# Kernel optimization log

Hardware: AMD Instinct MI355X
Metric: run time of the kernel (lower is better)

The kernel has to match this reference:

```python
import jax, jax.numpy as jnp
import numpy as np

B, C, H, W = 8, 512, 64, 64
NH = 8                 # num_heads
HD = C // NH           # head_dim = 64
WIN = 8 * 8            # tokens per window
NW = (H * W) // WIN    # number of windows = 64


def setup_inputs() -> dict:
    key = jax.random.key(0)
    ks = jax.random.split(key, 8)
    w = lambda k, shape: jax.random.normal(k, shape, jnp.float32) * 0.02
    return {
        "x": jax.random.normal(ks[0], (B, C, H, W), jnp.float32),
        "Wq": w(ks[1], (C, C)), "bq": jnp.zeros((C,), jnp.float32),
        "Wk": w(ks[2], (C, C)), "bk": jnp.zeros((C,), jnp.float32),
        "Wv": w(ks[3], (C, C)), "bv": jnp.zeros((C,), jnp.float32),
        "Bbias": w(ks[4], (WIN, WIN)),  # additive relative bias per (q,k) position in window
    }


def reference(x, Wq, bq, Wk, bk, Wv, bv, Bbias):
    shape = x.shape
    # (B, C, H, W) -> (B, n_windows, window, C)
    xw = x.reshape(shape[0], NW, WIN, C)
    # QKV projections (torch Linear: y = x @ W^T + b)
    q = (xw @ Wq.T + bq).reshape(B, NW, WIN, NH, HD).transpose(0, 1, 3, 2, 4)
    k = (xw @ Wk.T + bk).reshape(B, NW, WIN, NH, HD).transpose(0, 1, 3, 2, 4)
    v = (xw @ Wv.T + bv).reshape(B, NW, WIN, NH, HD).transpose(0, 1, 3, 2, 4)
    scale = 1.0 / jnp.sqrt(jnp.float32(HD))
    scores = jnp.einsum("bwhqd,bwhkd->bwhqk", q, k) * scale + Bbias  # bias broadcasts over b,w,h
    probs = jax.nn.softmax(scores, axis=-1)
    out = jnp.einsum("bwhqk,bwhkd->bwhqd", probs, v)
    out = out.transpose(0, 1, 3, 2, 4).reshape(shape)
    return out
```

## Files before the change

kernel.cpp:

```cpp
#include <hip/hip_runtime.h>
#include <hip/hip_bf16.h>


typedef __attribute__((ext_vector_type(8))) short bf16x8;
typedef __attribute__((ext_vector_type(4))) float f32x4;

#define GLDS(gp, lp) __builtin_amdgcn_global_load_lds( \
    (const __attribute__((address_space(1))) unsigned int*)(gp), \
    (__attribute__((address_space(3))) unsigned int*)(lp), 16, 0, 0)

__device__ __forceinline__ unsigned short f2bf(float f) {
  union { __hip_bfloat16 h; unsigned short u; } v;
  v.h = __float2bfloat16(f);
  return v.u;
}

__global__ __launch_bounds__(256) void prep_convert(
    const float* __restrict__ X, const float* __restrict__ Wq,
    const float* __restrict__ Wk, const float* __restrict__ Wv,
    unsigned short* __restrict__ Xb, unsigned short* __restrict__ Wc) {
  const unsigned int i = blockIdx.x * 256 + threadIdx.x;
  const float* src;
  unsigned short* dst;
  if (i < 2097152u) {
    src = X + (size_t)i * 8;
    dst = Xb + (size_t)i * 8;
  } else {
    const unsigned int j = i - 2097152u;
    const unsigned int e = j * 8;
    const unsigned int n = e >> 9, kk = e & 511;
    src = ((n < 512) ? Wq : (n < 1024 ? Wk : Wv)) + (size_t)(n & 511) * 512 + kk;
    dst = Wc + (size_t)n * 512 + kk;
  }
  float4 f0 = *(const float4*)(src);
  float4 f1 = *(const float4*)(src + 4);
  __align__(16) unsigned short u[8];
  u[0] = f2bf(f0.x); u[1] = f2bf(f0.y); u[2] = f2bf(f0.z); u[3] = f2bf(f0.w);
  u[4] = f2bf(f1.x); u[5] = f2bf(f1.y); u[6] = f2bf(f1.z); u[7] = f2bf(f1.w);
  *(bf16x8*)(dst) = *(const bf16x8*)(u);
}

__global__ __launch_bounds__(512, 2) void qkv_gemm_256(
    const unsigned short* __restrict__ Xb, const unsigned short* __restrict__ Wc,
    const float* __restrict__ bq, const float* __restrict__ bk,
    const float* __restrict__ bv,
    unsigned short* __restrict__ Qo, unsigned short* __restrict__ Ko,
    unsigned short* __restrict__ Vo) {
  __shared__ __align__(16) char LDS[131072];

  const int tid  = threadIdx.x;
  const int lane = tid & 63;
  const int wid  = tid >> 6;
  const int wm = wid >> 2, wn = wid & 3;

  const int work = (int)(blockIdx.x & 7) * 96 + (int)(blockIdx.x >> 3);
  const int bx = work % 6, by = work / 6;
  const int n0 = bx * 256, m0 = by * 256;

  const int lcol  = ((lane & 3) * 8) ^ ((lane >= 32) ? 16 : 0);
  const int arow0 = (wid >> 1) * 16 + (lane >> 2);
  const int acol0 = (wid & 1) * 32 + lcol;

#define STAGE_A(half, tt) do { \
    const unsigned short* g = Xb + (size_t)(m0 + (half) * 128 + arow0) * 512 + (tt) * 64 + acol0; \
    char* l = LDS + ((tt) & 1) * 32768 + (half) * 16384 + wid * 1024; \
    GLDS(g, l); \
    GLDS(g + 64 * 512, l + 8192); \
  } while (0)

#define STAGE_B(half, tt) do { \
    const unsigned short* g = Wc + (size_t)(n0 + (half) * 128 + arow0) * 512 + (tt) * 64 + acol0; \
    char* l = LDS + 65536 + ((tt) & 1) * 32768 + (half) * 16384 + wid * 1024; \
    GLDS(g, l); \
    GLDS(g + 64 * 512, l + 8192); \
  } while (0)

  const int sloff = (((lane & 15) * 64) + ((lane >> 4) * 16)) ^ ((lane & 8) ? 32 : 0);
  char* const Ab = LDS + wm * 16384 + sloff;
  char* const Bb2 = LDS + 65536 + (wn >> 1) * 16384 + sloff;
  const int bfr = (wn & 1) * 4;

  f32x4 acc[8][4];
#pragma unroll
  for (int i = 0; i < 8; ++i)
#pragma unroll
    for (int j = 0; j < 4; ++j) acc[i][j] = (f32x4){0.f, 0.f, 0.f, 0.f};

#define RD_A(dst, ks, bo) do { \
    _Pragma("unroll") for (int mi = 0; mi < 8; ++mi) \
      dst[mi] = *(const bf16x8*)(Ab + (bo) + mi * 2048 + (ks) * 1024); \
  } while (0)

#define RD_B(dst, ks, bo) do { \
    _Pragma("unroll") for (int ni = 0; ni < 4; ++ni) \
      dst[ni] = *(const bf16x8*)(Bb2 + (bo) + (bfr + ni) * 2048 + (ks) * 1024); \
  } while (0)

#define MMH(aa, bb) do { \
    _Pragma("unroll") for (int mi = 0; mi < 8; ++mi) \
    _Pragma("unroll") for (int ni = 0; ni < 4; ++ni) \
      acc[mi][ni] = __builtin_amdgcn_mfma_f32_16x16x32_bf16( \
          aa[mi], bb[ni], acc[mi][ni], 0, 0, 0); \
  } while (0)

  STAGE_A(0, 0); STAGE_A(1, 0); STAGE_B(0, 0); STAGE_B(1, 0);
  asm volatile("s_waitcnt vmcnt(0)" ::: "memory");
  __builtin_amdgcn_s_barrier();

  bf16x8 aP[8], bP[4], aQ[8], bQ[4];
  RD_A(aP, 0, 0); RD_B(bP, 0, 0);

  for (int t = 0; t < 8; ++t) {
    const int bo = (t & 1) * 32768;
    if (t + 1 < 8) {
      STAGE_A(0, t + 1); STAGE_A(1, t + 1);
      STAGE_B(0, t + 1); STAGE_B(1, t + 1);
    }
    RD_A(aQ, 1, bo); RD_B(bQ, 1, bo);
    MMH(aP, bP);
    MMH(aQ, bQ);
    if (t + 1 < 8) asm volatile("s_waitcnt vmcnt(0)" ::: "memory");
    __builtin_amdgcn_s_barrier();
    if (t + 1 < 8) { RD_A(aP, 0, bo ^ 32768); RD_B(bP, 0, bo ^ 32768); }
  }

  {
    const int p = n0 >> 9;
    const float* bias = (p == 0) ? bq : (p == 1) ? bk : bv;
    const float qs = (p == 0) ? 0.125f : 1.0f;
    const int hi = lane >> 4, lr = lane & 15;
    const int h = ((n0 & 511) + wn * 64) >> 6;
    char* const scr = LDS + wid * 8192;
    float bsv[4];
#pragma unroll
    for (int ni = 0; ni < 4; ++ni)
      bsv[ni] = bias[(n0 & 511) + wn * 64 + ni * 16 + lr];

#pragma unroll
    for (int wh = 0; wh < 2; ++wh) {
      asm volatile("s_waitcnt lgkmcnt(0)" ::: "memory");
      __builtin_amdgcn_sched_barrier(0);
      if (p < 2) {
#pragma unroll
        for (int f = 0; f < 4; ++f)
#pragma unroll
          for (int ni = 0; ni < 4; ++ni) {
            const int d = ni * 16 + lr;
#pragma unroll
            for (int rr = 0; rr < 4; ++rr) {
              const int t = f * 16 + hi * 4 + rr;
              const int off = t * 64 + (d ^ ((t & 7) << 3));
              *(unsigned short*)(scr + off * 2) =
                  f2bf((acc[wh * 4 + f][ni][rr] + bsv[ni]) * qs);
            }
          }
      } else {
#pragma unroll
        for (int f = 0; f < 4; ++f)
#pragma unroll
          for (int ni = 0; ni < 4; ++ni) {
            const int d = ni * 16 + lr;
            const int t0 = f * 16 + hi * 4;
            ushort4 pk;
            pk.x = f2bf(acc[wh * 4 + f][ni][0] + bsv[ni]);
            pk.y = f2bf(acc[wh * 4 + f][ni][1] + bsv[ni]);
            pk.z = f2bf(acc[wh * 4 + f][ni][2] + bsv[ni]);
            pk.w = f2bf(acc[wh * 4 + f][ni][3] + bsv[ni]);
            const int off = d * 64 + (t0 ^ ((d & 7) << 3));
            *(ushort4*)(scr + off * 2) = pk;
          }
      }
      asm volatile("s_waitcnt lgkmcnt(0)" ::: "memory");
      __builtin_amdgcn_sched_barrier(0);
      const int win = (m0 + wm * 128 + wh * 64) >> 6;
      unsigned short* dst =
          ((p == 0) ? Qo : (p == 1) ? Ko : Vo) + (size_t)(win * 8 + h) * 4096;
#pragma unroll
      for (int i = 0; i < 8; ++i) {
        const int r = i * 8 + (lane >> 3);
        const int c = lane & 7;
        const int off = r * 64 + ((c ^ (r & 7)) * 8);
        bf16x8 row = *(const bf16x8*)(scr + off * 2);
        *(bf16x8*)(dst + r * 64 + c * 8) = row;
      }
    }
  }
#undef STAGE_A
#undef STAGE_B
#undef RD_A
#undef RD_B
#undef MMH
}

__global__ __launch_bounds__(64) void attn_win(
    const unsigned short* __restrict__ Qp, const unsigned short* __restrict__ Kp,
    const unsigned short* __restrict__ Vp, const float* __restrict__ Bb,
    float* __restrict__ out) {
  __shared__ __align__(16) unsigned short P[64 * 72];
  const int lane = threadIdx.x;
  const int win = blockIdx.x >> 3;
  const int h   = blockIdx.x & 7;
  const size_t base = (size_t)(win * 8 + h) * 4096;
  const unsigned short* q = Qp + base;
  const unsigned short* k = Kp + base;
  const unsigned short* v = Vp + base;
  const int lr = lane & 15;
  const int hi = lane >> 4;

  bf16x8 qa[4][2], kb[4][2];
#pragma unroll
  for (int mt = 0; mt < 4; ++mt)
#pragma unroll
    for (int ks = 0; ks < 2; ++ks)
      qa[mt][ks] = *(const bf16x8*)(q + (size_t)(mt * 16 + lr) * 64 + ks * 32 + hi * 8);
#pragma unroll
  for (int nt = 0; nt < 4; ++nt)
#pragma unroll
    for (int ks = 0; ks < 2; ++ks)
      kb[nt][ks] = *(const bf16x8*)(k + (size_t)(nt * 16 + lr) * 64 + ks * 32 + hi * 8);

  f32x4 s[4][4];
#pragma unroll
  for (int mt = 0; mt < 4; ++mt)
#pragma unroll
    for (int nt = 0; nt < 4; ++nt) {
      s[mt][nt] = (f32x4){0.f, 0.f, 0.f, 0.f};
      s[mt][nt] = __builtin_amdgcn_mfma_f32_16x16x32_bf16(qa[mt][0], kb[nt][0], s[mt][nt], 0, 0, 0);
      s[mt][nt] = __builtin_amdgcn_mfma_f32_16x16x32_bf16(qa[mt][1], kb[nt][1], s[mt][nt], 0, 0, 0);
    }

#pragma unroll
  for (int mt = 0; mt < 4; ++mt)
#pragma unroll
    for (int nt = 0; nt < 4; ++nt)
#pragma unroll
      for (int rr = 0; rr < 4; ++rr)
        s[mt][nt][rr] += Bb[(mt * 16 + hi * 4 + rr) * 64 + nt * 16 + lr];

  float inv[4][4];
#pragma unroll
  for (int mt = 0; mt < 4; ++mt)
#pragma unroll
    for (int rr = 0; rr < 4; ++rr) {
      float m = fmaxf(fmaxf(s[mt][0][rr], s[mt][1][rr]),
                      fmaxf(s[mt][2][rr], s[mt][3][rr]));
      m = fmaxf(m, __shfl_xor(m, 1));
      m = fmaxf(m, __shfl_xor(m, 2));
      m = fmaxf(m, __shfl_xor(m, 4));
      m = fmaxf(m, __shfl_xor(m, 8));
      float sum = 0.f;
#pragma unroll
      for (int nt = 0; nt < 4; ++nt) {
        float e = __expf(s[mt][nt][rr] - m);
        s[mt][nt][rr] = e;
        sum += e;
      }
      sum += __shfl_xor(sum, 1);
      sum += __shfl_xor(sum, 2);
      sum += __shfl_xor(sum, 4);
      sum += __shfl_xor(sum, 8);
      inv[mt][rr] = 1.0f / sum;
    }

#pragma unroll
  for (int mt = 0; mt < 4; ++mt)
#pragma unroll
    for (int nt = 0; nt < 4; ++nt)
#pragma unroll
      for (int rr = 0; rr < 4; ++rr)
        P[(mt * 16 + hi * 4 + rr) * 72 + nt * 16 + lr] =
            f2bf(s[mt][nt][rr] * inv[mt][rr]);
  __syncthreads();

  bf16x8 pa[4][2], vb[4][2];
#pragma unroll
  for (int mt = 0; mt < 4; ++mt)
#pragma unroll
    for (int ks = 0; ks < 2; ++ks)
      pa[mt][ks] = *(const bf16x8*)(&P[(mt * 16 + lr) * 72 + ks * 32 + hi * 8]);
#pragma unroll
  for (int nt = 0; nt < 4; ++nt)
#pragma unroll
    for (int ks = 0; ks < 2; ++ks)
      vb[nt][ks] = *(const bf16x8*)(v + (size_t)(nt * 16 + lr) * 64 + ks * 32 + hi * 8);

  f32x4 o[4][4];
#pragma unroll
  for (int mt = 0; mt < 4; ++mt)
#pragma unroll
    for (int nt = 0; nt < 4; ++nt) {
      o[mt][nt] = (f32x4){0.f, 0.f, 0.f, 0.f};
      o[mt][nt] = __builtin_amdgcn_mfma_f32_16x16x32_bf16(pa[mt][0], vb[nt][0], o[mt][nt], 0, 0, 0);
      o[mt][nt] = __builtin_amdgcn_mfma_f32_16x16x32_bf16(pa[mt][1], vb[nt][1], o[mt][nt], 0, 0, 0);
    }

  float* op = out + (size_t)win * 32768 + h * 64;
#pragma unroll
  for (int mt = 0; mt < 4; ++mt)
#pragma unroll
    for (int nt = 0; nt < 4; ++nt)
#pragma unroll
      for (int rr = 0; rr < 4; ++rr)
        op[(size_t)(mt * 16 + hi * 4 + rr) * 512 + nt * 16 + lr] = o[mt][nt][rr];
}

extern "C" void kernel_launch(void* const* d_in, const int* in_sizes, int n_in,
                              void* d_out, int out_size, void* d_ws, size_t ws_size,
                              hipStream_t stream) {
  const float* x     = (const float*)d_in[0];
  const float* Wq    = (const float*)d_in[1];
  const float* bq    = (const float*)d_in[2];
  const float* Wk    = (const float*)d_in[3];
  const float* bk    = (const float*)d_in[4];
  const float* Wv    = (const float*)d_in[5];
  const float* bv    = (const float*)d_in[6];
  const float* Bbias = (const float*)d_in[7];
  float* out = (float*)d_out;

  unsigned short* Wc = (unsigned short*)d_ws;
  unsigned short* Xb = (unsigned short*)((char*)d_ws + ((size_t)2 << 20));
  unsigned short* Q  = (unsigned short*)((char*)d_ws + ((size_t)36 << 20));
  unsigned short* K  = (unsigned short*)((char*)d_ws + ((size_t)68 << 20));
  unsigned short* V  = (unsigned short*)((char*)d_ws + ((size_t)100 << 20));

  prep_convert<<<dim3(8576), dim3(256), 0, stream>>>(x, Wq, Wk, Wv, Xb, Wc);
  qkv_gemm_256<<<dim3(768), dim3(512), 0, stream>>>(Xb, Wc, bq, bk, bv, Q, K, V);
  attn_win<<<dim3(4096), dim3(64), 0, stream>>>(Q, K, V, Bbias, out);
}
```

Baseline: 112.3 us.

## Fuse fp32-to-bf16 conversion of X into the QKV GEMM A-tile load

Drops the separate pass that converted the whole X activation tensor to bf16 in workspace. The GEMM now loads fp32 X tiles into registers, converts them, and writes the swizzled bf16 tile into LDS after the MFMA phase, and only the weights are still pre-converted. This removes a full write and re-read of a 32 MB bf16 copy of X. In exchange the GEMM reads fp32 A data, which doubles its A bytes and re-reads it across the 6 N-tiles. The A path also moves from async global-to-LDS loads to register staging, and the register-level prefetch of the next k-slice fragments is dropped.

```diff
diff --git a/kernel.cpp b/kernel.cpp
--- a/kernel.cpp
+++ b/kernel.cpp
@@ -15,23 +15,14 @@
   return v.u;
 }
 
-__global__ __launch_bounds__(256) void prep_convert(
-    const float* __restrict__ X, const float* __restrict__ Wq,
-    const float* __restrict__ Wk, const float* __restrict__ Wv,
-    unsigned short* __restrict__ Xb, unsigned short* __restrict__ Wc) {
+__global__ __launch_bounds__(256) void prep_w(
+    const float* __restrict__ Wq, const float* __restrict__ Wk,
+    const float* __restrict__ Wv, unsigned short* __restrict__ Wc) {
   const unsigned int i = blockIdx.x * 256 + threadIdx.x;
-  const float* src;
-  unsigned short* dst;
-  if (i < 2097152u) {
-    src = X + (size_t)i * 8;
-    dst = Xb + (size_t)i * 8;
-  } else {
-    const unsigned int j = i - 2097152u;
-    const unsigned int e = j * 8;
-    const unsigned int n = e >> 9, kk = e & 511;
-    src = ((n < 512) ? Wq : (n < 1024 ? Wk : Wv)) + (size_t)(n & 511) * 512 + kk;
-    dst = Wc + (size_t)n * 512 + kk;
-  }
+  const unsigned int e = i * 8;
+  const unsigned int n = e >> 9, kk = e & 511;
+  const float* src = ((n < 512) ? Wq : (n < 1024 ? Wk : Wv)) + (size_t)(n & 511) * 512 + kk;
+  unsigned short* dst = Wc + (size_t)n * 512 + kk;
   float4 f0 = *(const float4*)(src);
   float4 f1 = *(const float4*)(src + 4);
   __align__(16) unsigned short u[8];
@@ -40,8 +31,8 @@
   *(bf16x8*)(dst) = *(const bf16x8*)(u);
 }
 
-__global__ __launch_bounds__(512, 2) void qkv_gemm_256(
-    const unsigned short* __restrict__ Xb, const unsigned short* __restrict__ Wc,
+__global__ __launch_bounds__(512, 2) void qkv_gemm_fx(
+    const float* __restrict__ X, const unsigned short* __restrict__ Wc,
     const float* __restrict__ bq, const float* __restrict__ bk,
     const float* __restrict__ bv,
     unsigned short* __restrict__ Qo, unsigned short* __restrict__ Ko,
@@ -57,22 +48,39 @@
   const int bx = work % 6, by = work / 6;
   const int n0 = bx * 256, m0 = by * 256;
 
+  const int ar  = tid >> 1;
+  const int aks = tid & 1;
+  const float* const ag = X + (size_t)(m0 + ar) * 512 + aks * 32;
+  char* const awr = LDS + (ar >> 7) * 16384 + ((ar & 127) >> 4) * 2048 +
+                    aks * 1024 + (ar & 15) * 64;
+  const int axor = (ar & 8) ? 32 : 0;
+
   const int lcol  = ((lane & 3) * 8) ^ ((lane >= 32) ? 16 : 0);
-  const int arow0 = (wid >> 1) * 16 + (lane >> 2);
-  const int acol0 = (wid & 1) * 32 + lcol;
-
-#define STAGE_A(half, tt) do { \
-    const unsigned short* g = Xb + (size_t)(m0 + (half) * 128 + arow0) * 512 + (tt) * 64 + acol0; \
-    char* l = LDS + ((tt) & 1) * 32768 + (half) * 16384 + wid * 1024; \
-    GLDS(g, l); \
-    GLDS(g + 64 * 512, l + 8192); \
-  } while (0)
+  const int brow0 = (wid >> 1) * 16 + (lane >> 2);
+  const int bcol0 = (wid & 1) * 32 + lcol;
 
 #define STAGE_B(half, tt) do { \
-    const unsigned short* g = Wc + (size_t)(n0 + (half) * 128 + arow0) * 512 + (tt) * 64 + acol0; \
+    const unsigned short* g = Wc + (size_t)(n0 + (half) * 128 + brow0) * 512 + (tt) * 64 + bcol0; \
     char* l = LDS + 65536 + ((tt) & 1) * 32768 + (half) * 16384 + wid * 1024; \
     GLDS(g, l); \
     GLDS(g + 64 * 512, l + 8192); \
+  } while (0)
+
+#define ALOAD(f, tt) do { \
+    _Pragma("unroll") for (int j = 0; j < 8; ++j) \
+      f[j] = *(const float4*)(ag + (tt) * 64 + j * 4); \
+  } while (0)
+
+#define AWRITE(f, tt) do { \
+    char* const wb = awr + ((tt) & 1) * 32768; \
+    _Pragma("unroll") for (int c = 0; c < 4; ++c) { \
+      __align__(16) unsigned short u[8]; \
+      u[0] = f2bf(f[2*c].x);   u[1] = f2bf(f[2*c].y); \
+      u[2] = f2bf(f[2*c].z);   u[3] = f2bf(f[2*c].w); \
+      u[4] = f2bf(f[2*c+1].x); u[5] = f2bf(f[2*c+1].y); \
+      u[6] = f2bf(f[2*c+1].z); u[7] = f2bf(f[2*c+1].w); \
+      *(bf16x8*)(wb + ((c * 16) ^ axor)) = *(const bf16x8*)(u); \
+    } \
   } while (0)
 
   const int sloff = (((lane & 15) * 64) + ((lane >> 4) * 16)) ^ ((lane & 8) ? 32 : 0);
@@ -103,25 +111,35 @@
           aa[mi], bb[ni], acc[mi][ni], 0, 0, 0); \
   } while (0)
 
-  STAGE_A(0, 0); STAGE_A(1, 0); STAGE_B(0, 0); STAGE_B(1, 0);
-  asm volatile("s_waitcnt vmcnt(0)" ::: "memory");
-  __builtin_amdgcn_s_barrier();
-
-  bf16x8 aP[8], bP[4], aQ[8], bQ[4];
-  RD_A(aP, 0, 0); RD_B(bP, 0, 0);
+  {
+    float4 f[8];
+    STAGE_B(0, 0); STAGE_B(1, 0);
+    ALOAD(f, 0);
+    AWRITE(f, 0);
+    asm volatile("s_waitcnt vmcnt(0) lgkmcnt(0)" ::: "memory");
+    __builtin_amdgcn_s_barrier();
+  }
 
   for (int t = 0; t < 8; ++t) {
     const int bo = (t & 1) * 32768;
+    float4 f[8];
     if (t + 1 < 8) {
-      STAGE_A(0, t + 1); STAGE_A(1, t + 1);
+      ALOAD(f, t + 1);
       STAGE_B(0, t + 1); STAGE_B(1, t + 1);
-    }
-    RD_A(aQ, 1, bo); RD_B(bQ, 1, bo);
-    MMH(aP, bP);
-    MMH(aQ, bQ);
-    if (t + 1 < 8) asm volatile("s_waitcnt vmcnt(0)" ::: "memory");
+      __builtin_amdgcn_sched_barrier(0);
+    }
+    {
+      bf16x8 a[8], b[4];
+      RD_A(a, 0, bo); RD_B(b, 0, bo);
+      MMH(a, b);
+      RD_A(a, 1, bo); RD_B(b, 1, bo);
+      MMH(a, b);
+    }
+    if (t + 1 < 8) {
+      AWRITE(f, t + 1);
+      asm volatile("s_waitcnt vmcnt(0) lgkmcnt(0)" ::: "memory");
+    }
     __builtin_amdgcn_s_barrier();
-    if (t + 1 < 8) { RD_A(aP, 0, bo ^ 32768); RD_B(bP, 0, bo ^ 32768); }
   }
 
   {
@@ -185,8 +203,9 @@
       }
     }
   }
-#undef STAGE_A
 #undef STAGE_B
+#undef ALOAD
+#undef AWRITE
 #undef RD_A
 #undef RD_B
 #undef MMH
@@ -318,12 +337,11 @@
   float* out = (float*)d_out;
 
   unsigned short* Wc = (unsigned short*)d_ws;
-  unsigned short* Xb = (unsigned short*)((char*)d_ws + ((size_t)2 << 20));
   unsigned short* Q  = (unsigned short*)((char*)d_ws + ((size_t)36 << 20));
   unsigned short* K  = (unsigned short*)((char*)d_ws + ((size_t)68 << 20));
   unsigned short* V  = (unsigned short*)((char*)d_ws + ((size_t)100 << 20));
 
-  prep_convert<<<dim3(8576), dim3(256), 0, stream>>>(x, Wq, Wk, Wv, Xb, Wc);
-  qkv_gemm_256<<<dim3(768), dim3(512), 0, stream>>>(Xb, Wc, bq, bk, bv, Q, K, V);
+  prep_w<<<dim3(384), dim3(256), 0, stream>>>(Wq, Wk, Wv, Wc);
+  qkv_gemm_fx<<<dim3(768), dim3(512), 0, stream>>>(x, Wc, bq, bk, bv, Q, K, V);
   attn_win<<<dim3(4096), dim3(64), 0, stream>>>(Q, K, V, Bbias, out);
 }
```

Result: slower. 140.3 us (+25.0%).

## Load GEMM A operand straight to registers, stage only B in LDS

Applied to the files above, without the earlier changes.

The QKV GEMM now reads the X tile from global memory directly into registers per wave, with a one-step prefetch across k-slices. Only the weight tile is staged through LDS via global_load_lds double buffering. This halves LDS use to 64 KB, which could allow two blocks per CU and removes the LDS write/read round trip for A. In exchange, the four waves sharing the same rows each fetch A separately, leaning on cache hits, and the global load latency for A sits closer to the MFMA chain.

```diff
diff --git a/kernel.cpp b/kernel.cpp
--- a/kernel.cpp
+++ b/kernel.cpp
@@ -40,13 +40,13 @@
   *(bf16x8*)(dst) = *(const bf16x8*)(u);
 }
 
-__global__ __launch_bounds__(512, 2) void qkv_gemm_256(
+__global__ __launch_bounds__(512, 2) void qkv_gemm_ad(
     const unsigned short* __restrict__ Xb, const unsigned short* __restrict__ Wc,
     const float* __restrict__ bq, const float* __restrict__ bk,
     const float* __restrict__ bv,
     unsigned short* __restrict__ Qo, unsigned short* __restrict__ Ko,
     unsigned short* __restrict__ Vo) {
-  __shared__ __align__(16) char LDS[131072];
+  __shared__ __align__(16) char LDS[65536];
 
   const int tid  = threadIdx.x;
   const int lane = tid & 63;
@@ -57,39 +57,28 @@
   const int bx = work % 6, by = work / 6;
   const int n0 = bx * 256, m0 = by * 256;
 
+  const unsigned short* const aG =
+      Xb + (size_t)(m0 + wm * 128 + (lane & 15)) * 512 + (lane >> 4) * 8;
+
+#define LD_A(dst, tt, ks) do { \
+    _Pragma("unroll") for (int mi = 0; mi < 8; ++mi) \
+      dst[mi] = *(const bf16x8*)(aG + (size_t)mi * 16 * 512 + (tt) * 64 + (ks) * 32); \
+  } while (0)
+
   const int lcol  = ((lane & 3) * 8) ^ ((lane >= 32) ? 16 : 0);
-  const int arow0 = (wid >> 1) * 16 + (lane >> 2);
-  const int acol0 = (wid & 1) * 32 + lcol;
-
-#define STAGE_A(half, tt) do { \
-    const unsigned short* g = Xb + (size_t)(m0 + (half) * 128 + arow0) * 512 + (tt) * 64 + acol0; \
+  const int brow0 = (wid >> 1) * 16 + (lane >> 2);
+  const int bcol0 = (wid & 1) * 32 + lcol;
+
+#define STAGE_B(half, tt) do { \
+    const unsigned short* g = Wc + (size_t)(n0 + (half) * 128 + brow0) * 512 + (tt) * 64 + bcol0; \
     char* l = LDS + ((tt) & 1) * 32768 + (half) * 16384 + wid * 1024; \
     GLDS(g, l); \
     GLDS(g + 64 * 512, l + 8192); \
   } while (0)
 
-#define STAGE_B(half, tt) do { \
-    const unsigned short* g = Wc + (size_t)(n0 + (half) * 128 + arow0) * 512 + (tt) * 64 + acol0; \
-    char* l = LDS + 65536 + ((tt) & 1) * 32768 + (half) * 16384 + wid * 1024; \
-    GLDS(g, l); \
-    GLDS(g + 64 * 512, l + 8192); \
-  } while (0)
-
   const int sloff = (((lane & 15) * 64) + ((lane >> 4) * 16)) ^ ((lane & 8) ? 32 : 0);
-  char* const Ab = LDS + wm * 16384 + sloff;
-  char* const Bb2 = LDS + 65536 + (wn >> 1) * 16384 + sloff;
+  char* const Bb2 = LDS + (wn >> 1) * 16384 + sloff;
   const int bfr = (wn & 1) * 4;
-
-  f32x4 acc[8][4];
-#pragma unroll
-  for (int i = 0; i < 8; ++i)
-#pragma unroll
-    for (int j = 0; j < 4; ++j) acc[i][j] = (f32x4){0.f, 0.f, 0.f, 0.f};
-
-#define RD_A(dst, ks, bo) do { \
-    _Pragma("unroll") for (int mi = 0; mi < 8; ++mi) \
-      dst[mi] = *(const bf16x8*)(Ab + (bo) + mi * 2048 + (ks) * 1024); \
-  } while (0)
 
 #define RD_B(dst, ks, bo) do { \
     _Pragma("unroll") for (int ni = 0; ni < 4; ++ni) \
@@ -103,25 +92,32 @@
           aa[mi], bb[ni], acc[mi][ni], 0, 0, 0); \
   } while (0)
 
-  STAGE_A(0, 0); STAGE_A(1, 0); STAGE_B(0, 0); STAGE_B(1, 0);
+  f32x4 acc[8][4];
+#pragma unroll
+  for (int i = 0; i < 8; ++i)
+#pragma unroll
+    for (int j = 0; j < 4; ++j) acc[i][j] = (f32x4){0.f, 0.f, 0.f, 0.f};
+
+  bf16x8 aC[8], aN[8], b[4];
+
+  STAGE_B(0, 0); STAGE_B(1, 0);
+  LD_A(aC, 0, 0);
   asm volatile("s_waitcnt vmcnt(0)" ::: "memory");
   __builtin_amdgcn_s_barrier();
-
-  bf16x8 aP[8], bP[4], aQ[8], bQ[4];
-  RD_A(aP, 0, 0); RD_B(bP, 0, 0);
 
   for (int t = 0; t < 8; ++t) {
     const int bo = (t & 1) * 32768;
     if (t + 1 < 8) {
-      STAGE_A(0, t + 1); STAGE_A(1, t + 1);
       STAGE_B(0, t + 1); STAGE_B(1, t + 1);
-    }
-    RD_A(aQ, 1, bo); RD_B(bQ, 1, bo);
-    MMH(aP, bP);
-    MMH(aQ, bQ);
-    if (t + 1 < 8) asm volatile("s_waitcnt vmcnt(0)" ::: "memory");
+      __builtin_amdgcn_sched_barrier(0);
+    }
+    LD_A(aN, t, 1);
+    RD_B(b, 0, bo);
+    MMH(aC, b);
+    if (t + 1 < 8) LD_A(aC, t + 1, 0);
+    RD_B(b, 1, bo);
+    MMH(aN, b);
     __builtin_amdgcn_s_barrier();
-    if (t + 1 < 8) { RD_A(aP, 0, bo ^ 32768); RD_B(bP, 0, bo ^ 32768); }
   }
 
   {
@@ -185,9 +181,8 @@
       }
     }
   }
-#undef STAGE_A
+#undef LD_A
 #undef STAGE_B
-#undef RD_A
 #undef RD_B
 #undef MMH
 }
@@ -324,6 +319,6 @@
   unsigned short* V  = (unsigned short*)((char*)d_ws + ((size_t)100 << 20));
 
   prep_convert<<<dim3(8576), dim3(256), 0, stream>>>(x, Wq, Wk, Wv, Xb, Wc);
-  qkv_gemm_256<<<dim3(768), dim3(512), 0, stream>>>(Xb, Wc, bq, bk, bv, Q, K, V);
+  qkv_gemm_ad<<<dim3(768), dim3(512), 0, stream>>>(Xb, Wc, bq, bk, bv, Q, K, V);
   attn_win<<<dim3(4096), dim3(64), 0, stream>>>(Q, K, V, Bbias, out);
 }
```

Measured after the change: 168.9 us. 1.5x slower.
